# Kernel tuning notes

Hardware: AMD Instinct MI355X
Metric: run time of the kernel (lower is better)

Reference implementation:

```python
import jax, jax.numpy as jnp
import numpy as np

N = 100000
E = 1600000
D_IN = 128
D_HID = 128
D_OUT = 128


def setup_inputs() -> dict:
    key = jax.random.key(0)
    k1, k2, k3, k4 = jax.random.split(key, 4)
    x_piece = jax.random.normal(k1, (N, D_IN), dtype=jnp.float32)
    edge_index_piece = jax.random.randint(k2, (2, E), 0, N, dtype=jnp.int64)
    # GCNConv parameters (Glorot-ish scale)
    W1 = jax.random.normal(k3, (D_IN, D_HID), dtype=jnp.float32) / np.sqrt(D_IN)
    b1 = jnp.zeros((D_HID,), dtype=jnp.float32)
    W2 = jax.random.normal(k4, (D_HID, D_OUT), dtype=jnp.float32) / np.sqrt(D_HID)
    b2 = jnp.zeros((D_OUT,), dtype=jnp.float32)
    return {"x_piece": x_piece, "edge_index_piece": edge_index_piece,
            "W1": W1, "b1": b1, "W2": W2, "b2": b2}


def gcn_conv(x, W, b, src, dst, n):
    """PyG GCNConv: out = D^-1/2 (A+I) D^-1/2 (x W) + b, with self-loops."""
    # x: [n, d_in], W: [d_in, d_out], src/dst: [E+n] (self-loops included)
    h = x @ W  # [n, d_out]
    deg = jax.ops.segment_sum(jnp.ones_like(dst, dtype=h.dtype), dst, num_segments=n)
    dinv = jnp.where(deg > 0, jax.lax.rsqrt(deg), 0.0)  # deg^-1/2
    norm = dinv[src] * dinv[dst]  # [E+n]
    msg = h[src] * norm[:, None]  # gather + normalize
    agg = jax.ops.segment_sum(msg, dst, num_segments=n)  # scatter-add
    return agg + b


def reference(x_piece, edge_index_piece, W1, b1, W2, b2):
    n = x_piece.shape[0]
    loops = jnp.arange(n, dtype=edge_index_piece.dtype)
    src = jnp.concatenate([edge_index_piece[0], loops])
    dst = jnp.concatenate([edge_index_piece[1], loops])
    h = gcn_conv(x_piece, W1, b1, src, dst, n)
    h = jax.nn.relu(h)
    out = gcn_conv(h, W2, b2, src, dst, n)
    return out
```

## Files before the change

kernel.cpp:

```cpp
#include <hip/hip_runtime.h>
#include <hip/hip_bf16.h>


#define D 128
#define BUKBITS 7
#define BUKSZ 128
#define MAXBUK 1024
#define SCHUNK 16384

typedef __attribute__((ext_vector_type(8))) short short8;
typedef __attribute__((ext_vector_type(4))) float f32x4;

static __device__ __forceinline__ ushort f2b(float f) {
    __hip_bfloat16 h = __float2bfloat16(f);
    return *reinterpret_cast<ushort*>(&h);
}


__global__ __launch_bounds__(256) void k_bukhist(const int* __restrict__ dst, int* __restrict__ bukcnt,
                                                 int E, int nbuk) {
    __shared__ int lh[MAXBUK];
    for (int i = threadIdx.x; i < nbuk; i += 256) lh[i] = 0;
    __syncthreads();
    int start = blockIdx.x * SCHUNK;
    int end = min(E, start + SCHUNK);
    for (int e = start + threadIdx.x; e < end; e += 256)
        atomicAdd(&lh[dst[e] >> BUKBITS], 1);
    __syncthreads();
    for (int i = threadIdx.x; i < nbuk; i += 256)
        if (lh[i]) atomicAdd(&bukcnt[i], lh[i]);
}

__global__ __launch_bounds__(256) void k_bukscan(const int* __restrict__ bukcnt, int* __restrict__ bukbase,
                                                 int* __restrict__ gcur, int nbuk, int E) {
    __shared__ int vals[MAXBUK];
    __shared__ int tsum[256];
    int t = threadIdx.x;
    for (int i = t; i < MAXBUK; i += 256) vals[i] = (i < nbuk) ? bukcnt[i] : 0;
    __syncthreads();
    int o = t * 4;
    int s = vals[o] + vals[o + 1] + vals[o + 2] + vals[o + 3];
    tsum[t] = s;
    __syncthreads();
    for (int off = 1; off < 256; off <<= 1) {
        int v = (t >= off) ? tsum[t - off] : 0;
        __syncthreads();
        tsum[t] += v;
        __syncthreads();
    }
    int run = tsum[t] - s;
    for (int i = 0; i < 4; i++) {
        int idx = o + i;
        if (idx < nbuk) { bukbase[idx] = run; gcur[idx] = run; }
        run += vals[idx];
    }
    if (t == 0) bukbase[nbuk] = E;
}

__global__ __launch_bounds__(256) void k_scatter(const int* __restrict__ src, const int* __restrict__ dst,
                                                 int* __restrict__ gcur, uint* __restrict__ tmp,
                                                 int E, int nbuk) {
    __shared__ int lh[MAXBUK];
    __shared__ int lbase[MAXBUK];
    for (int i = threadIdx.x; i < nbuk; i += 256) lh[i] = 0;
    __syncthreads();
    int start = blockIdx.x * SCHUNK;
    int end = min(E, start + SCHUNK);
    for (int e = start + threadIdx.x; e < end; e += 256)
        atomicAdd(&lh[dst[e] >> BUKBITS], 1);
    __syncthreads();
    for (int i = threadIdx.x; i < nbuk; i += 256) {
        int c = lh[i];
        lbase[i] = c ? atomicAdd(&gcur[i], c) : 0;
        lh[i] = 0;
    }
    __syncthreads();
    for (int e = start + threadIdx.x; e < end; e += 256) {
        int s = src[e];
        int d = dst[e];
        int bk = d >> BUKBITS;
        int r = atomicAdd(&lh[bk], 1);
        tmp[lbase[bk] + r] = ((uint)(d & (BUKSZ - 1)) << 25) | (uint)s;
    }
}

__global__ __launch_bounds__(256) void k_fillC(const uint* __restrict__ tmp, const int* __restrict__ bukbase,
                                               int* __restrict__ eord, int* __restrict__ rowptr,
                                               float* __restrict__ dinv, int n, int nbuk) {
    __shared__ int cnt[BUKSZ];
    __shared__ int sc[BUKSZ];
    __shared__ int lrp[BUKSZ];
    int b = blockIdx.x;
    int node0 = b << BUKBITS;
    int nn = min(BUKSZ, n - node0);
    int e0 = bukbase[b], e1 = bukbase[b + 1];
    int t = threadIdx.x;
    if (t < BUKSZ) cnt[t] = 0;
    __syncthreads();
    for (int e = e0 + t; e < e1; e += 256)
        atomicAdd(&cnt[tmp[e] >> 25], 1);
    __syncthreads();
    int c0 = (t < BUKSZ) ? cnt[t] : 0;
    if (t < BUKSZ) sc[t] = c0;
    __syncthreads();
    for (int off = 1; off < BUKSZ; off <<= 1) {
        int v = (t < BUKSZ && t >= off) ? sc[t - off] : 0;
        __syncthreads();
        if (t < BUKSZ) sc[t] += v;
        __syncthreads();
    }
    if (t < BUKSZ) lrp[t] = e0 + sc[t] - c0;
    if (t < nn) {
        rowptr[node0 + t] = e0 + sc[t] - c0;
        dinv[node0 + t] = 1.0f / sqrtf((float)(c0 + 1));
    }
    if (b == nbuk - 1 && t == 0) rowptr[n] = e1;
    __syncthreads();
    if (t < BUKSZ) cnt[t] = 0;
    __syncthreads();
    for (int e = e0 + t; e < e1; e += 256) {
        uint u = tmp[e];
        int dL = (int)(u >> 25);
        int s = (int)(u & 0x1FFFFFFu);
        int r = atomicAdd(&cnt[dL], 1);
        eord[lrp[dL] + r] = s;
    }
}

__global__ __launch_bounds__(256) void k_prepW(const float* __restrict__ W1, const float* __restrict__ W2,
                                               ushort* __restrict__ Wt1, ushort* __restrict__ Wt2) {
    int i = blockIdx.x * 256 + threadIdx.x;
    if (i < 16384) {
        int kk = i >> 7, nn = i & 127;
        Wt1[nn * 128 + kk] = f2b(W1[i]);
        Wt2[nn * 128 + kk] = f2b(W2[i]);
    }
}

__global__ __launch_bounds__(256) void k_gemm(const float* __restrict__ X, const ushort* __restrict__ Wt,
                                              ushort* __restrict__ Hb, int nrows) {
    const int wave = threadIdx.x >> 6;
    const int lane = threadIdx.x & 63;
    const int quad = lane >> 4;
    const int m = lane & 15;
    const int row0 = blockIdx.x * 64 + wave * 16;
    const int rowc = min(row0 + m, nrows - 1);

    f32x4 acc[8];
    #pragma unroll
    for (int t = 0; t < 8; t++) acc[t] = (f32x4){0.f, 0.f, 0.f, 0.f};

    #pragma unroll
    for (int ks = 0; ks < 4; ks++) {
        const int k0 = ks * 32 + quad * 8;
        const float* p = X + (size_t)rowc * D + k0;
        float4 u0 = ((const float4*)p)[0];
        float4 u1 = ((const float4*)p)[1];
        short8 a;
        a[0] = (short)f2b(u0.x); a[1] = (short)f2b(u0.y);
        a[2] = (short)f2b(u0.z); a[3] = (short)f2b(u0.w);
        a[4] = (short)f2b(u1.x); a[5] = (short)f2b(u1.y);
        a[6] = (short)f2b(u1.z); a[7] = (short)f2b(u1.w);
        #pragma unroll
        for (int t = 0; t < 8; t++) {
            short8 b = *(const short8*)(Wt + ((t * 16 + m) * D + k0));
            acc[t] = __builtin_amdgcn_mfma_f32_16x16x32_bf16(a, b, acc[t], 0, 0, 0);
        }
    }
    #pragma unroll
    for (int r = 0; r < 4; r++) {
        int orow = row0 + quad * 4 + r;
        if (orow < nrows) {
            #pragma unroll
            for (int t = 0; t < 8; t++)
                Hb[(size_t)orow * D + t * 16 + m] = f2b(acc[t][r]);
        }
    }
}

template <bool RELU>
__global__ __launch_bounds__(256) void k_agg(const ushort* __restrict__ Hb, const float* __restrict__ dinv,
                                             const int* __restrict__ rowptr, const int* __restrict__ eord,
                                             const float* __restrict__ bias, float* __restrict__ out, int n) {
    int v = blockIdx.x * 4 + (threadIdx.x >> 6);
    int lane = threadIdx.x & 63;
    if (v >= n) return;
    float dv = dinv[v];
    const uint* __restrict__ Hu = (const uint*)Hb;
    uint hs = Hu[(size_t)v * 64 + lane];
    float ax = dv * __uint_as_float(hs << 16);
    float ay = dv * __uint_as_float(hs & 0xffff0000u);
    int e = rowptr[v];
    const int end = rowptr[v + 1];
    for (; e + 7 < end; e += 8) {
        int s[8];
        #pragma unroll
        for (int i = 0; i < 8; i++) s[i] = eord[e + i];
        float w[8];
        uint h[8];
        #pragma unroll
        for (int i = 0; i < 8; i++) w[i] = dinv[s[i]];
        #pragma unroll
        for (int i = 0; i < 8; i++) h[i] = Hu[(size_t)s[i] * 64 + lane];
        #pragma unroll
        for (int i = 0; i < 8; i++) {
            ax += w[i] * __uint_as_float(h[i] << 16);
            ay += w[i] * __uint_as_float(h[i] & 0xffff0000u);
        }
    }
    for (; e + 3 < end; e += 4) {
        int s[4];
        #pragma unroll
        for (int i = 0; i < 4; i++) s[i] = eord[e + i];
        float w[4];
        uint h[4];
        #pragma unroll
        for (int i = 0; i < 4; i++) w[i] = dinv[s[i]];
        #pragma unroll
        for (int i = 0; i < 4; i++) h[i] = Hu[(size_t)s[i] * 64 + lane];
        #pragma unroll
        for (int i = 0; i < 4; i++) {
            ax += w[i] * __uint_as_float(h[i] << 16);
            ay += w[i] * __uint_as_float(h[i] & 0xffff0000u);
        }
    }
    for (; e < end; ++e) {
        int s = eord[e];
        float w = dinv[s];
        uint hh = Hu[(size_t)s * 64 + lane];
        ax += w * __uint_as_float(hh << 16);
        ay += w * __uint_as_float(hh & 0xffff0000u);
    }
    float2 bb = ((const float2*)bias)[lane];
    float rx = dv * ax + bb.x;
    float ry = dv * ay + bb.y;
    if (RELU) { rx = fmaxf(rx, 0.f); ry = fmaxf(ry, 0.f); }
    ((float2*)(out + (size_t)v * D))[lane] = make_float2(rx, ry);
}


static inline size_t alignup(size_t x) { return (x + 511) & ~(size_t)511; }

extern "C" void kernel_launch(void* const* d_in, const int* in_sizes, int n_in,
                              void* d_out, int out_size, void* d_ws, size_t ws_size,
                              hipStream_t stream) {
    const float* x  = (const float*)d_in[0];
    const int* eidx = (const int*)d_in[1];
    const float* W1 = (const float*)d_in[2];
    const float* b1 = (const float*)d_in[3];
    const float* W2 = (const float*)d_in[4];
    const float* b2 = (const float*)d_in[5];
    float* out = (float*)d_out;

    const int N = in_sizes[0] / D;
    const int E = in_sizes[1] / 2;
    const int* src = eidx;
    const int* dst = eidx + E;
    const int nbuk = (N + BUKSZ - 1) >> BUKBITS;

    char* ws = (char*)d_ws;
    size_t off = 0;
    int* bukcnt = (int*)(ws + off);   off = alignup(off + (size_t)MAXBUK * 4);
    int* bukbase = (int*)(ws + off);  off = alignup(off + (size_t)(MAXBUK + 1) * 4);
    int* gcur   = (int*)(ws + off);   off = alignup(off + (size_t)MAXBUK * 4);
    int* rowptr = (int*)(ws + off);   off = alignup(off + (size_t)(N + 1) * 4);
    float* dinv = (float*)(ws + off); off = alignup(off + (size_t)N * 4);
    int* eord   = (int*)(ws + off);   off = alignup(off + (size_t)E * 4);
    ushort* hbuf = (ushort*)(ws + off); off = alignup(off + (size_t)N * D * 2);
    ushort* Wt1 = (ushort*)(ws + off); off = alignup(off + 16384 * 2);
    ushort* Wt2 = (ushort*)(ws + off); off = alignup(off + 16384 * 2);
    uint* tmp = (uint*)hbuf;
    (void)ws_size;

    const int nT = 256;
    const int gChunk = (E + SCHUNK - 1) / SCHUNK;

    hipMemsetAsync(bukcnt, 0, (size_t)MAXBUK * 4, stream);
    k_prepW<<<64, nT, 0, stream>>>(W1, W2, Wt1, Wt2);
    k_bukhist<<<gChunk, nT, 0, stream>>>(dst, bukcnt, E, nbuk);
    k_bukscan<<<1, nT, 0, stream>>>(bukcnt, bukbase, gcur, nbuk, E);
    k_scatter<<<gChunk, nT, 0, stream>>>(src, dst, gcur, tmp, E, nbuk);
    k_fillC<<<nbuk, nT, 0, stream>>>(tmp, bukbase, eord, rowptr, dinv, N, nbuk);

    const int gGemm = (N + 63) / 64;
    const int gAgg = (N + 3) / 4;

    k_gemm<<<gGemm, nT, 0, stream>>>(x, Wt1, hbuf, N);
    k_agg<true><<<gAgg, nT, 0, stream>>>(hbuf, dinv, rowptr, eord, b1, out, N);

    k_gemm<<<gGemm, nT, 0, stream>>>(out, Wt2, hbuf, N);
    k_agg<false><<<gAgg, nT, 0, stream>>>(hbuf, dinv, rowptr, eord, b2, out, N);
}
```

Baseline: 379.1 us.

## Pre-scale GEMM rows by dinv and store layer-one activations as bf16

The GEMM epilogue now multiplies each output row by its source dinv. This lets the aggregation kernel drop the per-edge dinv gather and multiply, and its edge loop is unrolled to 16. Layer one writes its ReLU output as bf16 into a new workspace buffer, and the second GEMM reads bf16 directly, which halves that intermediate's traffic. The cost is an extra bf16 rounding of the hidden activations and a larger workspace.

```diff
diff --git a/kernel.cpp b/kernel.cpp
--- a/kernel.cpp
+++ b/kernel.cpp
@@ -137,8 +137,10 @@
     }
 }
 
-__global__ __launch_bounds__(256) void k_gemm(const float* __restrict__ X, const ushort* __restrict__ Wt,
-                                              ushort* __restrict__ Hb, int nrows) {
+template <bool ABF16>
+__global__ __launch_bounds__(256) void k_gemm(const void* __restrict__ Xv, const ushort* __restrict__ Wt,
+                                              const float* __restrict__ dinv, ushort* __restrict__ Hb,
+                                              int nrows) {
     const int wave = threadIdx.x >> 6;
     const int lane = threadIdx.x & 63;
     const int quad = lane >> 4;
@@ -153,14 +155,18 @@
     #pragma unroll
     for (int ks = 0; ks < 4; ks++) {
         const int k0 = ks * 32 + quad * 8;
-        const float* p = X + (size_t)rowc * D + k0;
-        float4 u0 = ((const float4*)p)[0];
-        float4 u1 = ((const float4*)p)[1];
         short8 a;
-        a[0] = (short)f2b(u0.x); a[1] = (short)f2b(u0.y);
-        a[2] = (short)f2b(u0.z); a[3] = (short)f2b(u0.w);
-        a[4] = (short)f2b(u1.x); a[5] = (short)f2b(u1.y);
-        a[6] = (short)f2b(u1.z); a[7] = (short)f2b(u1.w);
+        if (ABF16) {
+            a = *(const short8*)((const ushort*)Xv + (size_t)rowc * D + k0);
+        } else {
+            const float* p = (const float*)Xv + (size_t)rowc * D + k0;
+            float4 u0 = ((const float4*)p)[0];
+            float4 u1 = ((const float4*)p)[1];
+            a[0] = (short)f2b(u0.x); a[1] = (short)f2b(u0.y);
+            a[2] = (short)f2b(u0.z); a[3] = (short)f2b(u0.w);
+            a[4] = (short)f2b(u1.x); a[5] = (short)f2b(u1.y);
+            a[6] = (short)f2b(u1.z); a[7] = (short)f2b(u1.w);
+        }
         #pragma unroll
         for (int t = 0; t < 8; t++) {
             short8 b = *(const short8*)(Wt + ((t * 16 + m) * D + k0));
@@ -171,71 +177,69 @@
     for (int r = 0; r < 4; r++) {
         int orow = row0 + quad * 4 + r;
         if (orow < nrows) {
+            float dvv = dinv[orow];
             #pragma unroll
             for (int t = 0; t < 8; t++)
-                Hb[(size_t)orow * D + t * 16 + m] = f2b(acc[t][r]);
-        }
-    }
-}
-
-template <bool RELU>
+                Hb[(size_t)orow * D + t * 16 + m] = f2b(acc[t][r] * dvv);
+        }
+    }
+}
+
+template <bool RELU, bool OBF16>
 __global__ __launch_bounds__(256) void k_agg(const ushort* __restrict__ Hb, const float* __restrict__ dinv,
                                              const int* __restrict__ rowptr, const int* __restrict__ eord,
-                                             const float* __restrict__ bias, float* __restrict__ out, int n) {
+                                             const float* __restrict__ bias, void* __restrict__ outp, int n) {
     int v = blockIdx.x * 4 + (threadIdx.x >> 6);
     int lane = threadIdx.x & 63;
     if (v >= n) return;
     float dv = dinv[v];
     const uint* __restrict__ Hu = (const uint*)Hb;
     uint hs = Hu[(size_t)v * 64 + lane];
-    float ax = dv * __uint_as_float(hs << 16);
-    float ay = dv * __uint_as_float(hs & 0xffff0000u);
+    float ax = __uint_as_float(hs << 16);
+    float ay = __uint_as_float(hs & 0xffff0000u);
     int e = rowptr[v];
     const int end = rowptr[v + 1];
-    for (; e + 7 < end; e += 8) {
-        int s[8];
-        #pragma unroll
-        for (int i = 0; i < 8; i++) s[i] = eord[e + i];
-        float w[8];
-        uint h[8];
-        #pragma unroll
-        for (int i = 0; i < 8; i++) w[i] = dinv[s[i]];
-        #pragma unroll
-        for (int i = 0; i < 8; i++) h[i] = Hu[(size_t)s[i] * 64 + lane];
-        #pragma unroll
-        for (int i = 0; i < 8; i++) {
-            ax += w[i] * __uint_as_float(h[i] << 16);
-            ay += w[i] * __uint_as_float(h[i] & 0xffff0000u);
+    for (; e + 15 < end; e += 16) {
+        int s[16];
+        #pragma unroll
+        for (int i = 0; i < 16; i++) s[i] = eord[e + i];
+        uint h[16];
+        #pragma unroll
+        for (int i = 0; i < 16; i++) h[i] = Hu[(size_t)s[i] * 64 + lane];
+        #pragma unroll
+        for (int i = 0; i < 16; i++) {
+            ax += __uint_as_float(h[i] << 16);
+            ay += __uint_as_float(h[i] & 0xffff0000u);
         }
     }
     for (; e + 3 < end; e += 4) {
         int s[4];
         #pragma unroll
         for (int i = 0; i < 4; i++) s[i] = eord[e + i];
-        float w[4];
         uint h[4];
         #pragma unroll
-        for (int i = 0; i < 4; i++) w[i] = dinv[s[i]];
-        #pragma unroll
         for (int i = 0; i < 4; i++) h[i] = Hu[(size_t)s[i] * 64 + lane];
         #pragma unroll
         for (int i = 0; i < 4; i++) {
-            ax += w[i] * __uint_as_float(h[i] << 16);
-            ay += w[i] * __uint_as_float(h[i] & 0xffff0000u);
+            ax += __uint_as_float(h[i] << 16);
+            ay += __uint_as_float(h[i] & 0xffff0000u);
         }
     }
     for (; e < end; ++e) {
-        int s = eord[e];
-        float w = dinv[s];
-        uint hh = Hu[(size_t)s * 64 + lane];
-        ax += w * __uint_as_float(hh << 16);
-        ay += w * __uint_as_float(hh & 0xffff0000u);
+        uint hh = Hu[(size_t)eord[e] * 64 + lane];
+        ax += __uint_as_float(hh << 16);
+        ay += __uint_as_float(hh & 0xffff0000u);
     }
     float2 bb = ((const float2*)bias)[lane];
     float rx = dv * ax + bb.x;
     float ry = dv * ay + bb.y;
     if (RELU) { rx = fmaxf(rx, 0.f); ry = fmaxf(ry, 0.f); }
-    ((float2*)(out + (size_t)v * D))[lane] = make_float2(rx, ry);
+    if (OBF16) {
+        uint w = ((uint)f2b(ry) << 16) | (uint)f2b(rx);
+        ((uint*)outp)[(size_t)v * 64 + lane] = w;
+    } else {
+        ((float2*)((float*)outp + (size_t)v * D))[lane] = make_float2(rx, ry);
+    }
 }
 
 
@@ -267,6 +271,7 @@
     float* dinv = (float*)(ws + off); off = alignup(off + (size_t)N * 4);
     int* eord   = (int*)(ws + off);   off = alignup(off + (size_t)E * 4);
     ushort* hbuf = (ushort*)(ws + off); off = alignup(off + (size_t)N * D * 2);
+    ushort* act  = (ushort*)(ws + off); off = alignup(off + (size_t)N * D * 2);
     ushort* Wt1 = (ushort*)(ws + off); off = alignup(off + 16384 * 2);
     ushort* Wt2 = (ushort*)(ws + off); off = alignup(off + 16384 * 2);
     uint* tmp = (uint*)hbuf;
@@ -285,9 +290,9 @@
     const int gGemm = (N + 63) / 64;
     const int gAgg = (N + 3) / 4;
 
-    k_gemm<<<gGemm, nT, 0, stream>>>(x, Wt1, hbuf, N);
-    k_agg<true><<<gAgg, nT, 0, stream>>>(hbuf, dinv, rowptr, eord, b1, out, N);
-
-    k_gemm<<<gGemm, nT, 0, stream>>>(out, Wt2, hbuf, N);
-    k_agg<false><<<gAgg, nT, 0, stream>>>(hbuf, dinv, rowptr, eord, b2, out, N);
-}
+    k_gemm<false><<<gGemm, nT, 0, stream>>>((const void*)x, Wt1, dinv, hbuf, N);
+    k_agg<true, true><<<gAgg, nT, 0, stream>>>(hbuf, dinv, rowptr, eord, b1, (void*)act, N);
+
+    k_gemm<true><<<gGemm, nT, 0, stream>>>((const void*)act, Wt2, dinv, hbuf, N);
+    k_agg<false, false><<<gAgg, nT, 0, stream>>>(hbuf, dinv, rowptr, eord, b2, (void*)out, N);
+}
```

After: 368.9 us. 1.03x faster.
